# Performance work log

Hardware: AMD Instinct MI355X
Metric: run time of the kernel (lower is better)

## Reference

```python
import jax, jax.numpy as jnp
import numpy as np

WS = (2, 7, 7)          # window size (s, h, w)
DIM = 192
HEADS = 6
HEAD_DIM = DIM // HEADS
N = WS[0] * WS[1] * WS[2]  # 98
TABLE = (2 * WS[0] - 1) * (2 * WS[1] - 1) * (2 * WS[2] - 1)  # 507


def _relative_position_index():
    coords = np.stack(np.meshgrid(np.arange(WS[0]), np.arange(WS[1]), np.arange(WS[2]), indexing='ij'))
    cf = coords.reshape(3, -1)                      # [3, N]
    rel = cf[:, :, None] - cf[:, None, :]           # [3, N, N]
    rel = rel.transpose(1, 2, 0).astype(np.int64)   # [N, N, 3]
    rel[..., 0] += WS[0] - 1
    rel[..., 1] += WS[1] - 1
    rel[..., 2] += WS[2] - 1
    rel[..., 0] *= 3 * WS[1] - 1  # faithful to source (quirky multiplier)
    rel[..., 1] *= 2 * WS[1] - 1
    return jnp.asarray(rel.sum(-1), dtype=jnp.int32)  # [N, N]


def setup_inputs() -> dict:
    key = jax.random.key(0)
    ks = jax.random.split(key, 8)
    B_ = 1024
    nW = 64
    skip = jax.random.normal(ks[0], (B_, N, DIM), dtype=jnp.float32)
    x_up = jax.random.normal(ks[1], (B_, N, DIM), dtype=jnp.float32)
    mask = jax.random.normal(ks[2], (nW, N, N), dtype=jnp.float32)
    kv_w = jax.random.normal(ks[3], (DIM, 2 * DIM), dtype=jnp.float32) * 0.02
    kv_b = jnp.zeros((2 * DIM,), dtype=jnp.float32)
    proj_w = jax.random.normal(ks[4], (DIM, DIM), dtype=jnp.float32) * 0.02
    proj_b = jnp.zeros((DIM,), dtype=jnp.float32)
    rpb_table = jax.random.normal(ks[5], (TABLE, HEADS), dtype=jnp.float32) * 0.02
    rel_idx = _relative_position_index()
    return {"skip": skip, "x_up": x_up, "mask": mask, "kv_w": kv_w, "kv_b": kv_b,
            "proj_w": proj_w, "proj_b": proj_b, "rpb_table": rpb_table, "rel_idx": rel_idx}


def reference(skip, x_up, mask, kv_w, kv_b, proj_w, proj_b, rpb_table, rel_idx):
    B_, n, C = skip.shape
    nW = mask.shape[0]
    scale = HEAD_DIM ** -0.5
    kv = skip @ kv_w + kv_b                                # [B_, N, 2C]
    kv = kv.reshape(B_, n, 2, HEADS, HEAD_DIM)
    k = kv[:, :, 0]                                        # [B_, N, H, hd]
    v = kv[:, :, 1]
    q = x_up.reshape(B_, n, HEADS, HEAD_DIM) * scale
    attn = jnp.einsum('bqhd,bkhd->bhqk', q, k)             # [B_, H, N, N]
    bias = rpb_table[rel_idx]                              # [N, N, H]
    attn = attn + jnp.transpose(bias, (2, 0, 1))[None]
    attn = attn.reshape(B_ // nW, nW, HEADS, n, n) + mask[None, :, None]
    attn = attn.reshape(B_, HEADS, n, n)
    attn = jax.nn.softmax(attn, axis=-1)
    out = jnp.einsum('bhqk,bkhd->bqhd', attn, v).reshape(B_, n, C)
    return out @ proj_w + proj_b
```

## Files before the change

### kernel.cpp

```cpp
#include <hip/hip_runtime.h>
#include <hip/hip_bf16.h>

#define NTOK 98
#define DIM 192
#define HEADS 6
#define SCALE 0.17677669529663687f

using shortx8 = __attribute__((ext_vector_type(8))) short;
using floatx4 = __attribute__((ext_vector_type(4))) float;

static __device__ __forceinline__ unsigned short f2bf(float f) {
    unsigned u = __float_as_uint(f);
    u += 0x7FFFu + ((u >> 16) & 1u);
    return (unsigned short)(u >> 16);
}

static __device__ __forceinline__ shortx8 pack8(const float* p, float scale) {
    float4 a = *(const float4*)p;
    float4 b = *(const float4*)(p + 4);
    shortx8 t;
    t[0] = (short)f2bf(a.x * scale); t[1] = (short)f2bf(a.y * scale);
    t[2] = (short)f2bf(a.z * scale); t[3] = (short)f2bf(a.w * scale);
    t[4] = (short)f2bf(b.x * scale); t[5] = (short)f2bf(b.y * scale);
    t[6] = (short)f2bf(b.z * scale); t[7] = (short)f2bf(b.w * scale);
    return t;
}

__global__ void prep_kernel(const float* __restrict__ rpb, const int* __restrict__ relidx,
                            const float* __restrict__ kvw, const float* __restrict__ pw,
                            float* __restrict__ biasF, unsigned short* __restrict__ kvB,
                            unsigned short* __restrict__ pB) {
    int e = blockIdx.x * 256 + threadIdx.x;
    if (e < HEADS * NTOK * NTOK) {
        int h = e / (NTOK * NTOK), ij = e % (NTOK * NTOK);
        biasF[e] = rpb[relidx[ij] * HEADS + h];
    }
    if (e < 73728) {
        int jj = e & 7, lane = (e >> 3) & 63, t = e >> 9;
        int NT = t % 24, ks = t / 24;
        int c = ks * 32 + (lane >> 4) * 8 + jj;
        int n = NT * 16 + (lane & 15);
        kvB[e] = f2bf(kvw[c * 384 + n]);
    }
    if (e < 36864) {
        int jj = e & 7, lane = (e >> 3) & 63, t = e >> 9;
        int NT = t % 12, ks = t / 12;
        int c = ks * 32 + (lane >> 4) * 8 + jj;
        int n = NT * 16 + (lane & 15);
        pB[e] = f2bf(pw[c * 192 + n]);
    }
}

__global__ __launch_bounds__(448, 4) void attn_kernel(
    const float* __restrict__ skip, const float* __restrict__ xup,
    const float* __restrict__ mask, const float* __restrict__ kv_b,
    const float* __restrict__ biasF, const unsigned short* __restrict__ kvB,
    float* __restrict__ o_out) {

    __shared__ unsigned short kB3[3 * 7 * 512];
    __shared__ unsigned short vB3[3 * 2 * 4 * 512];
    __shared__ unsigned short PA[7 * 4 * 512];

    const int tid  = threadIdx.x;
    const int w    = tid >> 6;
    const int lane = tid & 63;
    const int l15  = lane & 15;
    const int quad = lane >> 4;
    const int win  = blockIdx.x >> 1;
    const int g    = blockIdx.x & 1;

    for (int e = tid; e < 6 * 512; e += 448)
        vB3[(e / 512) * 4 * 512 + 3 * 512 + (e & 511)] = 0;
    for (int e = tid; e < 7 * 256; e += 448)
        PA[(e / 256) * 4 * 512 + 3 * 512 + 256 + (e & 255)] = 0;
    __syncthreads();

    const int mA  = w * 16 + l15;
    const int mAc = mA < NTOK ? mA : 97;

    shortx8 afr[6];
    {
        const float* sr = skip + ((size_t)win * NTOK + mAc) * DIM + quad * 8;
        #pragma unroll
        for (int ks = 0; ks < 6; ++ks) afr[ks] = pack8(sr + ks * 32, 1.0f);
    }
    #pragma unroll
    for (int nt = 0; nt < 12; ++nt) {
        const int NTg = (nt < 6) ? (6 * g + nt) : (6 + 6 * g + nt);
        const int col = NTg * 16 + l15;
        const float cb = kv_b[col];
        floatx4 acc = {cb, cb, cb, cb};
        #pragma unroll
        for (int ks = 0; ks < 6; ++ks) {
            shortx8 bf = *(const shortx8*)(kvB + ((size_t)((ks * 24 + NTg) * 64 + lane)) * 8);
            acc = __builtin_amdgcn_mfma_f32_16x16x32_bf16(afr[ks], bf, acc, 0, 0, 0);
        }
        if (nt < 6) {
            const int ch = nt * 16 + l15, hh = ch >> 5, dh = ch & 31;
            const int base = ((hh * 7 + w) * 64) * 8 + (dh & 7);
            const int lphi = ((dh >> 3) & 3) << 4;
            #pragma unroll
            for (int r = 0; r < 4; ++r) {
                int mm = quad * 4 + r;
                kB3[base + (mm | lphi) * 8] = f2bf(acc[r]);
            }
        } else {
            const int cv = (nt - 6) * 16 + l15, hh = cv >> 5, dh = cv & 31, ntv = dh >> 4;
            #pragma unroll
            for (int r = 0; r < 4; ++r) {
                int m = w * 16 + quad * 4 + r;
                if (m < NTOK) {
                    int lp = (dh & 15) | (((m >> 3) & 3) << 4);
                    vB3[(((hh * 2 + ntv) * 4 + (m >> 5)) * 64 + lp) * 8 + (m & 7)] = f2bf(acc[r]);
                }
            }
        }
    }
    __syncthreads();

    const float* mw = mask + (size_t)(win & 63) * NTOK * NTOK;

    for (int hp = 0; hp < 3; ++hp) {
        const int h = 3 * g + hp;
        shortx8 qf;
        {
            const float* xr = xup + ((size_t)win * NTOK + mAc) * DIM + h * 32 + quad * 8;
            qf = pack8(xr, SCALE);
        }
        floatx4 S[7];
        const float* bh = biasF + h * NTOK * NTOK;
        #pragma unroll
        for (int nt = 0; nt < 7; ++nt) {
            const int j = nt * 16 + l15;
            #pragma unroll
            for (int r = 0; r < 4; ++r) {
                int i = w * 16 + quad * 4 + r;
                int ic = i < NTOK ? i : 97;
                S[nt][r] = (j < NTOK) ? (bh[ic * NTOK + j] + mw[ic * NTOK + j]) : -1e30f;
            }
        }
        #pragma unroll
        for (int nt = 0; nt < 7; ++nt) {
            shortx8 bk = *(const shortx8*)&kB3[((hp * 7 + nt) * 64 + lane) * 8];
            S[nt] = __builtin_amdgcn_mfma_f32_16x16x32_bf16(qf, bk, S[nt], 0, 0, 0);
        }
        float inv[4];
        #pragma unroll
        for (int r = 0; r < 4; ++r) {
            float mx = S[0][r];
            #pragma unroll
            for (int nt = 1; nt < 7; ++nt) mx = fmaxf(mx, S[nt][r]);
            mx = fmaxf(mx, __shfl_xor(mx, 1));
            mx = fmaxf(mx, __shfl_xor(mx, 2));
            mx = fmaxf(mx, __shfl_xor(mx, 4));
            mx = fmaxf(mx, __shfl_xor(mx, 8));
            float sm = 0.f;
            #pragma unroll
            for (int nt = 0; nt < 7; ++nt) { float ev = __expf(S[nt][r] - mx); S[nt][r] = ev; sm += ev; }
            sm += __shfl_xor(sm, 1);
            sm += __shfl_xor(sm, 2);
            sm += __shfl_xor(sm, 4);
            sm += __shfl_xor(sm, 8);
            inv[r] = 1.0f / sm;
        }
        #pragma unroll
        for (int nt = 0; nt < 7; ++nt) {
            const int j = nt * 16 + l15;
            const int ks = nt >> 1;
            const int lphi = ((j >> 3) & 3) << 4;
            #pragma unroll
            for (int r = 0; r < 4; ++r) {
                int mm = quad * 4 + r;
                PA[((w * 4 + ks) * 64 + (mm | lphi)) * 8 + (j & 7)] = f2bf(S[nt][r] * inv[r]);
            }
        }
        __syncthreads();
        shortx8 pa[4];
        #pragma unroll
        for (int ks = 0; ks < 4; ++ks)
            pa[ks] = *(const shortx8*)&PA[((w * 4 + ks) * 64 + lane) * 8];
        #pragma unroll
        for (int nt = 0; nt < 2; ++nt) {
            floatx4 o = {0.f, 0.f, 0.f, 0.f};
            #pragma unroll
            for (int ks = 0; ks < 4; ++ks) {
                shortx8 vb = *(const shortx8*)&vB3[(((hp * 2 + nt) * 4 + ks) * 64 + lane) * 8];
                o = __builtin_amdgcn_mfma_f32_16x16x32_bf16(pa[ks], vb, o, 0, 0, 0);
            }
            #pragma unroll
            for (int r = 0; r < 4; ++r) {
                int m = w * 16 + quad * 4 + r;
                if (m < NTOK)
                    o_out[((size_t)win * NTOK + m) * DIM + h * 32 + nt * 16 + l15] = o[r];
            }
        }
        __syncthreads();
    }
}

__global__ __launch_bounds__(448, 4) void proj_kernel(
    float* __restrict__ io, const unsigned short* __restrict__ pB,
    const float* __restrict__ pb) {
    const int tid  = threadIdx.x;
    const int w    = tid >> 6;
    const int lane = tid & 63;
    const int l15  = lane & 15;
    const int quad = lane >> 4;
    const int win  = blockIdx.x;

    float* base = io + (size_t)win * NTOK * DIM;
    const int mA  = w * 16 + l15;
    const int mAc = mA < NTOK ? mA : 97;

    shortx8 afr[6];
    {
        const float* ar = base + mAc * DIM + quad * 8;
        #pragma unroll
        for (int ks = 0; ks < 6; ++ks) afr[ks] = pack8(ar + ks * 32, 1.0f);
    }
    #pragma unroll
    for (int nt = 0; nt < 12; ++nt) {
        const int n = nt * 16 + l15;
        const float bb = pb[n];
        floatx4 acc = {bb, bb, bb, bb};
        #pragma unroll
        for (int ks = 0; ks < 6; ++ks) {
            shortx8 bf = *(const shortx8*)(pB + ((size_t)((ks * 12 + nt) * 64 + lane)) * 8);
            acc = __builtin_amdgcn_mfma_f32_16x16x32_bf16(afr[ks], bf, acc, 0, 0, 0);
        }
        #pragma unroll
        for (int r = 0; r < 4; ++r) {
            int m = w * 16 + quad * 4 + r;
            if (m < NTOK) base[m * DIM + n] = acc[r];
        }
    }
}

extern "C" void kernel_launch(void* const* d_in, const int* in_sizes, int n_in,
                              void* d_out, int out_size, void* d_ws, size_t ws_size,
                              hipStream_t stream) {
    const float* skip   = (const float*)d_in[0];
    const float* x_up   = (const float*)d_in[1];
    const float* mask   = (const float*)d_in[2];
    const float* kv_w   = (const float*)d_in[3];
    const float* kv_b   = (const float*)d_in[4];
    const float* proj_w = (const float*)d_in[5];
    const float* proj_b = (const float*)d_in[6];
    const float* rpb    = (const float*)d_in[7];
    const int*   relidx = (const int*)d_in[8];
    float* out = (float*)d_out;

    float*          biasF = (float*)d_ws;
    unsigned short* kvB   = (unsigned short*)((char*)d_ws + 230496);
    unsigned short* pB    = (unsigned short*)((char*)d_ws + 377952);

    prep_kernel<<<288, 256, 0, stream>>>(rpb, relidx, kv_w, proj_w, biasF, kvB, pB);
    attn_kernel<<<2048, 448, 0, stream>>>(skip, x_up, mask, kv_b, biasF, kvB, out);
    proj_kernel<<<1024, 448, 0, stream>>>(out, pB, proj_b);
}
```

Baseline: 336.8 us.

## Fuse attention and output projection into one per-window kernel

```diff
diff --git a/kernel.cpp b/kernel.cpp
--- a/kernel.cpp
+++ b/kernel.cpp
@@ -1,5 +1,4 @@
 #include <hip/hip_runtime.h>
-#include <hip/hip_bf16.h>
 
 #define NTOK 98
 #define DIM 192
@@ -51,29 +50,31 @@
     }
 }
 
-__global__ __launch_bounds__(448, 4) void attn_kernel(
+__global__ __launch_bounds__(448, 4) void fused_kernel(
     const float* __restrict__ skip, const float* __restrict__ xup,
     const float* __restrict__ mask, const float* __restrict__ kv_b,
     const float* __restrict__ biasF, const unsigned short* __restrict__ kvB,
-    float* __restrict__ o_out) {
-
-    __shared__ unsigned short kB3[3 * 7 * 512];
-    __shared__ unsigned short vB3[3 * 2 * 4 * 512];
-    __shared__ unsigned short PA[7 * 4 * 512];
+    const unsigned short* __restrict__ pB, const float* __restrict__ pb,
+    float* __restrict__ out) {
+
+    __shared__ __align__(16) unsigned short lds[29696];
+    unsigned short* kB  = lds;
+    unsigned short* vB  = lds + 7168;
+    unsigned short* PAb = lds + 15360;
 
     const int tid  = threadIdx.x;
     const int w    = tid >> 6;
     const int lane = tid & 63;
     const int l15  = lane & 15;
     const int quad = lane >> 4;
-    const int win  = blockIdx.x >> 1;
-    const int g    = blockIdx.x & 1;
-
-    for (int e = tid; e < 6 * 512; e += 448)
-        vB3[(e / 512) * 4 * 512 + 3 * 512 + (e & 511)] = 0;
+    const int win  = blockIdx.x;
+
+    for (int e = tid; e < 2048; e += 448) {
+        int pt = e >> 9, off = e & 511;
+        vB[pt * 2048 + 3 * 512 + off] = 0;
+    }
     for (int e = tid; e < 7 * 256; e += 448)
-        PA[(e / 256) * 4 * 512 + 3 * 512 + 256 + (e & 255)] = 0;
-    __syncthreads();
+        PAb[(e / 256) * 2048 + 3 * 512 + 256 + (e & 255)] = 0;
 
     const int mA  = w * 16 + l15;
     const int mAc = mA < NTOK ? mA : 97;
@@ -84,49 +85,65 @@
         #pragma unroll
         for (int ks = 0; ks < 6; ++ks) afr[ks] = pack8(sr + ks * 32, 1.0f);
     }
-    #pragma unroll
-    for (int nt = 0; nt < 12; ++nt) {
-        const int NTg = (nt < 6) ? (6 * g + nt) : (6 + 6 * g + nt);
-        const int col = NTg * 16 + l15;
-        const float cb = kv_b[col];
-        floatx4 acc = {cb, cb, cb, cb};
-        #pragma unroll
-        for (int ks = 0; ks < 6; ++ks) {
-            shortx8 bf = *(const shortx8*)(kvB + ((size_t)((ks * 24 + NTg) * 64 + lane)) * 8);
-            acc = __builtin_amdgcn_mfma_f32_16x16x32_bf16(afr[ks], bf, acc, 0, 0, 0);
-        }
-        if (nt < 6) {
-            const int ch = nt * 16 + l15, hh = ch >> 5, dh = ch & 31;
-            const int base = ((hh * 7 + w) * 64) * 8 + (dh & 7);
+
+    const float* mw = mask + (size_t)(win & 63) * NTOK * NTOK;
+    unsigned opk[12][2];
+
+    #pragma unroll
+    for (int h = 0; h < 6; ++h) {
+        const int p = h & 1;
+
+        shortx8 qf = pack8(xup + ((size_t)win * NTOK + mAc) * DIM + h * 32 + quad * 8, SCALE);
+
+        floatx4 ak[2], av[2];
+        #pragma unroll
+        for (int t = 0; t < 2; ++t) {
+            const int NT = 2 * h + t;
+            const float cb = kv_b[NT * 16 + l15];
+            floatx4 acc = {cb, cb, cb, cb};
+            #pragma unroll
+            for (int ks = 0; ks < 6; ++ks) {
+                shortx8 bf = *(const shortx8*)(kvB + ((size_t)((ks * 24 + NT) * 64 + lane)) * 8);
+                acc = __builtin_amdgcn_mfma_f32_16x16x32_bf16(afr[ks], bf, acc, 0, 0, 0);
+            }
+            ak[t] = acc;
+        }
+        #pragma unroll
+        for (int t = 0; t < 2; ++t) {
+            const int NT = 12 + 2 * h + t;
+            const float cb = kv_b[NT * 16 + l15];
+            floatx4 acc = {cb, cb, cb, cb};
+            #pragma unroll
+            for (int ks = 0; ks < 6; ++ks) {
+                shortx8 bf = *(const shortx8*)(kvB + ((size_t)((ks * 24 + NT) * 64 + lane)) * 8);
+                acc = __builtin_amdgcn_mfma_f32_16x16x32_bf16(afr[ks], bf, acc, 0, 0, 0);
+            }
+            av[t] = acc;
+        }
+        #pragma unroll
+        for (int t = 0; t < 2; ++t) {
+            const int dh = t * 16 + l15;
+            const int base = p * 3584 + (w * 64) * 8 + (dh & 7);
             const int lphi = ((dh >> 3) & 3) << 4;
             #pragma unroll
             for (int r = 0; r < 4; ++r) {
                 int mm = quad * 4 + r;
-                kB3[base + (mm | lphi) * 8] = f2bf(acc[r]);
-            }
-        } else {
-            const int cv = (nt - 6) * 16 + l15, hh = cv >> 5, dh = cv & 31, ntv = dh >> 4;
+                kB[base + (mm | lphi) * 8] = f2bf(ak[t][r]);
+            }
+        }
+        #pragma unroll
+        for (int t = 0; t < 2; ++t) {
             #pragma unroll
             for (int r = 0; r < 4; ++r) {
                 int m = w * 16 + quad * 4 + r;
                 if (m < NTOK) {
-                    int lp = (dh & 15) | (((m >> 3) & 3) << 4);
-                    vB3[(((hh * 2 + ntv) * 4 + (m >> 5)) * 64 + lp) * 8 + (m & 7)] = f2bf(acc[r]);
+                    int lp = l15 | (((m >> 3) & 3) << 4);
+                    vB[p * 4096 + ((t * 4 + (m >> 5)) * 64 + lp) * 8 + (m & 7)] = f2bf(av[t][r]);
                 }
             }
         }
-    }
-    __syncthreads();
-
-    const float* mw = mask + (size_t)(win & 63) * NTOK * NTOK;
-
-    for (int hp = 0; hp < 3; ++hp) {
-        const int h = 3 * g + hp;
-        shortx8 qf;
-        {
-            const float* xr = xup + ((size_t)win * NTOK + mAc) * DIM + h * 32 + quad * 8;
-            qf = pack8(xr, SCALE);
-        }
+        __syncthreads();
+
         floatx4 S[7];
         const float* bh = biasF + h * NTOK * NTOK;
         #pragma unroll
@@ -141,7 +158,7 @@
         }
         #pragma unroll
         for (int nt = 0; nt < 7; ++nt) {
-            shortx8 bk = *(const shortx8*)&kB3[((hp * 7 + nt) * 64 + lane) * 8];
+            shortx8 bk = *(const shortx8*)&kB[p * 3584 + (nt * 64 + lane) * 8];
             S[nt] = __builtin_amdgcn_mfma_f32_16x16x32_bf16(qf, bk, S[nt], 0, 0, 0);
         }
         float inv[4];
@@ -171,53 +188,49 @@
             #pragma unroll
             for (int r = 0; r < 4; ++r) {
                 int mm = quad * 4 + r;
-                PA[((w * 4 + ks) * 64 + (mm | lphi)) * 8 + (j & 7)] = f2bf(S[nt][r] * inv[r]);
+                PAb[((w * 4 + ks) * 64 + (mm | lphi)) * 8 + (j & 7)] = f2bf(S[nt][r]);
             }
         }
         __syncthreads();
+
         shortx8 pa[4];
         #pragma unroll
         for (int ks = 0; ks < 4; ++ks)
-            pa[ks] = *(const shortx8*)&PA[((w * 4 + ks) * 64 + lane) * 8];
+            pa[ks] = *(const shortx8*)&PAb[((w * 4 + ks) * 64 + lane) * 8];
         #pragma unroll
         for (int nt = 0; nt < 2; ++nt) {
             floatx4 o = {0.f, 0.f, 0.f, 0.f};
             #pragma unroll
             for (int ks = 0; ks < 4; ++ks) {
-                shortx8 vb = *(const shortx8*)&vB3[(((hp * 2 + nt) * 4 + ks) * 64 + lane) * 8];
+                shortx8 vb = *(const shortx8*)&vB[p * 4096 + ((nt * 4 + ks) * 64 + lane) * 8];
                 o = __builtin_amdgcn_mfma_f32_16x16x32_bf16(pa[ks], vb, o, 0, 0, 0);
             }
-            #pragma unroll
-            for (int r = 0; r < 4; ++r) {
-                int m = w * 16 + quad * 4 + r;
-                if (m < NTOK)
-                    o_out[((size_t)win * NTOK + m) * DIM + h * 32 + nt * 16 + l15] = o[r];
-            }
-        }
-        __syncthreads();
-    }
-}
-
-__global__ __launch_bounds__(448, 4) void proj_kernel(
-    float* __restrict__ io, const unsigned short* __restrict__ pB,
-    const float* __restrict__ pb) {
-    const int tid  = threadIdx.x;
-    const int w    = tid >> 6;
-    const int lane = tid & 63;
-    const int l15  = lane & 15;
-    const int quad = lane >> 4;
-    const int win  = blockIdx.x;
-
-    float* base = io + (size_t)win * NTOK * DIM;
-    const int mA  = w * 16 + l15;
-    const int mAc = mA < NTOK ? mA : 97;
-
-    shortx8 afr[6];
-    {
-        const float* ar = base + mAc * DIM + quad * 8;
-        #pragma unroll
-        for (int ks = 0; ks < 6; ++ks) afr[ks] = pack8(ar + ks * 32, 1.0f);
-    }
+            opk[h * 2 + nt][0] = (unsigned)f2bf(o[0] * inv[0]) | ((unsigned)f2bf(o[1] * inv[1]) << 16);
+            opk[h * 2 + nt][1] = (unsigned)f2bf(o[2] * inv[2]) | ((unsigned)f2bf(o[3] * inv[3]) << 16);
+        }
+    }
+
+    __syncthreads();
+
+    #pragma unroll
+    for (int h = 0; h < 6; ++h)
+        #pragma unroll
+        for (int nt = 0; nt < 2; ++nt)
+            #pragma unroll
+            for (int r = 0; r < 4; ++r) {
+                int mm = quad * 4 + r;
+                int dsub = nt * 16 + l15;
+                unsigned v = opk[h * 2 + nt][r >> 1] >> ((r & 1) * 16);
+                lds[((w * 6 + h) * 64 + (mm | (((dsub >> 3) & 3) << 4))) * 8 + (dsub & 7)] =
+                    (unsigned short)v;
+            }
+    __syncthreads();
+
+    shortx8 oa[6];
+    #pragma unroll
+    for (int ks = 0; ks < 6; ++ks)
+        oa[ks] = *(const shortx8*)&lds[((w * 6 + ks) * 64 + lane) * 8];
+    float* obase = out + (size_t)win * NTOK * DIM;
     #pragma unroll
     for (int nt = 0; nt < 12; ++nt) {
         const int n = nt * 16 + l15;
@@ -226,12 +239,12 @@
         #pragma unroll
         for (int ks = 0; ks < 6; ++ks) {
             shortx8 bf = *(const shortx8*)(pB + ((size_t)((ks * 12 + nt) * 64 + lane)) * 8);
-            acc = __builtin_amdgcn_mfma_f32_16x16x32_bf16(afr[ks], bf, acc, 0, 0, 0);
+            acc = __builtin_amdgcn_mfma_f32_16x16x32_bf16(oa[ks], bf, acc, 0, 0, 0);
         }
         #pragma unroll
         for (int r = 0; r < 4; ++r) {
             int m = w * 16 + quad * 4 + r;
-            if (m < NTOK) base[m * DIM + n] = acc[r];
+            if (m < NTOK) obase[m * DIM + n] = acc[r];
         }
     }
 }
@@ -255,6 +268,5 @@
     unsigned short* pB    = (unsigned short*)((char*)d_ws + 377952);
 
     prep_kernel<<<288, 256, 0, stream>>>(rpb, relidx, kv_w, proj_w, biasF, kvB, pB);
-    attn_kernel<<<2048, 448, 0, stream>>>(skip, x_up, mask, kv_b, biasF, kvB, out);
-    proj_kernel<<<1024, 448, 0, stream>>>(out, pB, proj_b);
-}
+    fused_kernel<<<1024, 448, 0, stream>>>(skip, x_up, mask, kv_b, biasF, kvB, pB, proj_b, out);
+}
```

Result: slower. 634.0 us (+88.3%).
